# Kernel tuning notes

Measured on AMD Instinct MI355X. Metric: run time of the kernel, lower is better.

## Reference

```python
import jax, jax.numpy as jnp
import numpy as np

D, H, KVH, HD, FF = 768, 12, 4, 64, 2048
N_REP = H // KVH
EPS = 1e-6


def rmsnorm(x, w):
    # Faithful to source: norm = ||x|| * n^{-1/2}; eps added to norm (not inside sqrt)
    norm = jnp.sqrt(jnp.sum(x * x, axis=-1, keepdims=True)) * (x.shape[-1] ** -0.5)
    return w * x / (norm + EPS)


def rope_tables(seq_len, head_dim, base=10000.0):
    inv_freq = 1.0 / (base ** (np.arange(0, head_dim, 2, dtype=np.float32) / head_dim))
    t = np.arange(seq_len, dtype=np.float32)
    freqs = np.einsum('i,j->ij', t, inv_freq)  # [S, HD/2]
    emb = np.concatenate([freqs, freqs], axis=-1)  # [S, HD]
    return jnp.asarray(np.cos(emb)), jnp.asarray(np.sin(emb))


def rotate_half(x):
    h = x.shape[-1] // 2
    return jnp.concatenate([-x[..., h:], x[..., :h]], axis=-1)


def setup_inputs() -> dict:
    key = jax.random.key(0)
    ks = jax.random.split(key, 9)
    s = 0.02
    return {
        'x': jax.random.normal(ks[0], (2, 2048, D), jnp.float32),
        'Wq': jax.random.normal(ks[1], (H * HD, D), jnp.float32) * s,
        'Wk': jax.random.normal(ks[2], (KVH * HD, D), jnp.float32) * s,
        'Wv': jax.random.normal(ks[3], (KVH * HD, D), jnp.float32) * s,
        'Wo': jax.random.normal(ks[4], (D, H * HD), jnp.float32) * s,
        'Wgate': jax.random.normal(ks[5], (FF, D), jnp.float32) * s,
        'Wup': jax.random.normal(ks[6], (FF, D), jnp.float32) * s,
        'Wdown': jax.random.normal(ks[7], (D, FF), jnp.float32) * s,
        'g1': jnp.ones((D,), jnp.float32),
        'g2': jnp.ones((D,), jnp.float32),
    }


def reference(x, Wq, Wk, Wv, Wo, Wgate, Wup, Wdown, g1, g2):
    B, S, _ = x.shape
    # ---- attention sublayer (pre-norm) ----
    xn = rmsnorm(x, g1)
    q = (xn @ Wq.T).reshape(B, S, H, HD).transpose(0, 2, 1, 3)      # [B,H,S,HD]
    k = (xn @ Wk.T).reshape(B, S, KVH, HD).transpose(0, 2, 1, 3)    # [B,KVH,S,HD]
    v = (xn @ Wv.T).reshape(B, S, KVH, HD).transpose(0, 2, 1, 3)
    cos, sin = rope_tables(S, HD)                                   # [S,HD]
    q = q * cos + rotate_half(q) * sin
    k = k * cos + rotate_half(k) * sin
    # repeat kv heads to match q heads
    k = jnp.repeat(k, N_REP, axis=1)                                # [B,H,S,HD]
    v = jnp.repeat(v, N_REP, axis=1)
    scores = jnp.einsum('bhqd,bhkd->bhqk', q, k) / jnp.sqrt(jnp.float32(HD))
    causal = jnp.tril(jnp.ones((S, S), bool))
    scores = jnp.where(causal, scores, jnp.finfo(scores.dtype).min)
    attn = jax.nn.softmax(scores, axis=-1)
    out = jnp.einsum('bhqk,bhkd->bhqd', attn, v)                    # [B,H,S,HD]
    out = out.transpose(0, 2, 1, 3).reshape(B, S, H * HD) @ Wo.T
    x = x + out
    # ---- SwiGLU FFN sublayer (pre-norm) ----
    xn2 = rmsnorm(x, g2)
    ff = (jax.nn.silu(xn2 @ Wgate.T) * (xn2 @ Wup.T)) @ Wdown.T
    return x + ff
```

## Files before the change

kernel.cpp:

```cpp
#include <hip/hip_runtime.h>
#include <hip/hip_bf16.h>
#include <math.h>

typedef __bf16 bf16;
typedef __attribute__((ext_vector_type(8))) __bf16 bf16x8;
typedef __attribute__((ext_vector_type(4))) __bf16 bf16x4;
typedef __attribute__((ext_vector_type(4))) float f32x4;

#define MFMA16(a,b,c) __builtin_amdgcn_mfma_f32_16x16x32_bf16(a,b,c,0,0,0)

#define BATCH 2
#define SEQ   2048
#define DMODEL 768
#define NH    12
#define NKV   4
#define NREP  3
#define HD    64
#define FFDIM 2048
#define ROWS  (BATCH*SEQ)

#define QSCALE 0.18033688011112042f
#define LOG2E  1.4426950408889634f

__device__ __forceinline__ void gl2lds16(const bf16* g, bf16* l) {
  __builtin_amdgcn_global_load_lds(
      (const __attribute__((address_space(1))) void*)g,
      (__attribute__((address_space(3))) void*)l, 16, 0, 0);
}

struct Cvt7 { const float* s[7]; bf16* d[7]; int n[7]; };
__global__ __launch_bounds__(256) void cvt_all_kernel(Cvt7 c) {
  int seg = blockIdx.y;
  const float* __restrict__ src = c.s[seg];
  bf16* __restrict__ dst = c.d[seg];
  int n = c.n[seg];
  int stride = gridDim.x * 256;
  for (int i = blockIdx.x * 256 + threadIdx.x; i < n; i += stride)
    dst[i] = (bf16)src[i];
}

__global__ __launch_bounds__(256) void rmsnorm_kernel(const float* __restrict__ x,
    const float* __restrict__ g, bf16* __restrict__ out) {
  int row = blockIdx.x;
  const float* xr = x + (size_t)row * DMODEL;
  int t = threadIdx.x;
  float v0 = xr[t], v1 = xr[t + 256], v2 = xr[t + 512];
  float ss = v0 * v0 + v1 * v1 + v2 * v2;
  #pragma unroll
  for (int off = 32; off; off >>= 1) ss += __shfl_xor(ss, off, 64);
  __shared__ float red[4];
  if ((t & 63) == 0) red[t >> 6] = ss;
  __syncthreads();
  float total = red[0] + red[1] + red[2] + red[3];
  float norm = sqrtf(total) * 0.03608439182435161f;
  float sc = 1.0f / (norm + 1e-6f);
  bf16* orow = out + (size_t)row * DMODEL;
  orow[t]       = (bf16)(g[t]       * v0 * sc);
  orow[t + 256] = (bf16)(g[t + 256] * v1 * sc);
  orow[t + 512] = (bf16)(g[t + 512] * v2 * sc);
}

template<bool RES, typename OUTT>
__global__ __launch_bounds__(256) void gemm_bt64_kernel(const bf16* __restrict__ A,
    const bf16* __restrict__ B, OUTT* __restrict__ C, const float* __restrict__ R,
    int N, int K) {
  __shared__ __align__(16) bf16 At[64 * 32];
  __shared__ __align__(16) bf16 Bt[128 * 32];
  int t = threadIdx.x;
  int lane = t & 63;
  int wave = t >> 6;
  int l15 = lane & 15, lq = lane >> 4;
  int wrow = (wave >> 1) * 32, wcol = (wave & 1) * 64;
  int row0 = blockIdx.y * 64;
  int col0 = blockIdx.x * 128;
  int srow = t >> 2, sseg = (t & 3) * 8;
  const bf16* Ag0 = A + (size_t)(row0 + srow) * K + sseg;
  const bf16* Bg0 = B + (size_t)(col0 + srow) * K + sseg;
  const bf16* Bg1 = Bg0 + (size_t)64 * K;
  bf16* Al0 = At + t * 8;
  bf16* Bl0 = Bt + t * 8;
  bf16* Bl1 = Bt + 2048 + t * 8;

  f32x4 zero = {0.f, 0.f, 0.f, 0.f};
  f32x4 acc[2][4];
  #pragma unroll
  for (int m = 0; m < 2; ++m)
    #pragma unroll
    for (int n = 0; n < 4; ++n) acc[m][n] = zero;

  for (int k0 = 0; k0 < K; k0 += 32) {
    __syncthreads();
    gl2lds16(Ag0 + k0, Al0);
    gl2lds16(Bg0 + k0, Bl0);
    gl2lds16(Bg1 + k0, Bl1);
    __syncthreads();
    bf16x8 af[2], bf[4];
    #pragma unroll
    for (int m = 0; m < 2; ++m)
      af[m] = *(const bf16x8*)(At + (wrow + m * 16 + l15) * 32 + lq * 8);
    #pragma unroll
    for (int n = 0; n < 4; ++n)
      bf[n] = *(const bf16x8*)(Bt + (wcol + n * 16 + l15) * 32 + lq * 8);
    #pragma unroll
    for (int m = 0; m < 2; ++m)
      #pragma unroll
      for (int n = 0; n < 4; ++n)
        acc[m][n] = MFMA16(af[m], bf[n], acc[m][n]);
  }
  #pragma unroll
  for (int m = 0; m < 2; ++m)
    #pragma unroll
    for (int n = 0; n < 4; ++n)
      #pragma unroll
      for (int r = 0; r < 4; ++r) {
        size_t idx = (size_t)(row0 + wrow + m * 16 + lq * 4 + r) * N
                   + (col0 + wcol + n * 16 + l15);
        float v = acc[m][n][r];
        if (RES) v += R[idx];
        C[idx] = (OUTT)v;
      }
}

__global__ __launch_bounds__(256) void gemm_gu_kernel(const bf16* __restrict__ A,
    const bf16* __restrict__ Wg, const bf16* __restrict__ Wu, bf16* __restrict__ H) {
  __shared__ __align__(16) bf16 At[128 * 32];
  __shared__ __align__(16) bf16 Bgt[64 * 32];
  __shared__ __align__(16) bf16 But[64 * 32];
  const int K = DMODEL;
  int t = threadIdx.x;
  int lane = t & 63, wave = t >> 6;
  int l15 = lane & 15, lq = lane >> 4;
  int wrow = (wave >> 1) * 64, wcol = (wave & 1) * 32;
  int row0 = blockIdx.y * 128;
  int col0 = blockIdx.x * 64;
  int srow = t >> 2, sseg = (t & 3) * 8;
  const bf16* Ag0 = A + (size_t)(row0 + srow) * K + sseg;
  const bf16* Ag1 = Ag0 + (size_t)64 * K;
  const bf16* Gg = Wg + (size_t)(col0 + srow) * K + sseg;
  const bf16* Ug = Wu + (size_t)(col0 + srow) * K + sseg;
  bf16* Al0 = At + t * 8;
  bf16* Al1 = At + 2048 + t * 8;
  bf16* Bgd = Bgt + t * 8;
  bf16* Bud = But + t * 8;

  f32x4 zero = {0.f, 0.f, 0.f, 0.f};
  f32x4 ag[4][2], au[4][2];
  #pragma unroll
  for (int m = 0; m < 4; ++m)
    #pragma unroll
    for (int n = 0; n < 2; ++n) { ag[m][n] = zero; au[m][n] = zero; }

  for (int k0 = 0; k0 < K; k0 += 32) {
    __syncthreads();
    gl2lds16(Ag0 + k0, Al0);
    gl2lds16(Ag1 + k0, Al1);
    gl2lds16(Gg + k0, Bgd);
    gl2lds16(Ug + k0, Bud);
    __syncthreads();
    bf16x8 af[4], bg[2], bu[2];
    #pragma unroll
    for (int m = 0; m < 4; ++m)
      af[m] = *(const bf16x8*)(At + (wrow + m * 16 + l15) * 32 + lq * 8);
    #pragma unroll
    for (int n = 0; n < 2; ++n) {
      bg[n] = *(const bf16x8*)(Bgt + (wcol + n * 16 + l15) * 32 + lq * 8);
      bu[n] = *(const bf16x8*)(But + (wcol + n * 16 + l15) * 32 + lq * 8);
    }
    #pragma unroll
    for (int m = 0; m < 4; ++m)
      #pragma unroll
      for (int n = 0; n < 2; ++n) {
        ag[m][n] = MFMA16(af[m], bg[n], ag[m][n]);
        au[m][n] = MFMA16(af[m], bu[n], au[m][n]);
      }
  }
  #pragma unroll
  for (int m = 0; m < 4; ++m)
    #pragma unroll
    for (int n = 0; n < 2; ++n)
      #pragma unroll
      for (int r = 0; r < 4; ++r) {
        int row = row0 + wrow + m * 16 + lq * 4 + r;
        int col = col0 + wcol + n * 16 + l15;
        float g = ag[m][n][r], u = au[m][n][r];
        float sg = g / (1.f + __builtin_amdgcn_exp2f(-g * LOG2E));
        H[(size_t)row * FFDIM + col] = (bf16)(sg * u);
      }
}

__global__ __launch_bounds__(64) void rope_kernel(const bf16* __restrict__ qkv,
    bf16* __restrict__ Qh, bf16* __restrict__ Kh, bf16* __restrict__ Vt) {
  int token = blockIdx.x;
  int b = token >> 11, s = token & (SEQ - 1);
  int d = threadIdx.x;
  int j = d & 31;
  float inv = expf(-(float)j * (9.210340371976184f / 32.0f));
  float ang = (float)s * inv;
  float c = cosf(ang), si = sinf(ang);
  float sgn = (d < 32) ? -1.f : 1.f;
  const bf16* qr = qkv + (size_t)token * 1280;
  #pragma unroll
  for (int h = 0; h < NH; ++h) {
    float v = (float)qr[h * 64 + d];
    float other = (float)qr[h * 64 + (d ^ 32)];
    Qh[((size_t)(b * NH + h) * SEQ + s) * 64 + d] = (bf16)((v * c + sgn * other * si) * QSCALE);
  }
  #pragma unroll
  for (int hk = 0; hk < NKV; ++hk) {
    float v = (float)qr[768 + hk * 64 + d];
    float other = (float)qr[768 + hk * 64 + (d ^ 32)];
    Kh[((size_t)(b * NKV + hk) * SEQ + s) * 64 + d] = (bf16)(v * c + sgn * other * si);
    float vv = (float)qr[1024 + hk * 64 + d];
    Vt[((size_t)(b * NKV + hk) * 64 + d) * SEQ + s] = (bf16)vv;
  }
}

__global__ __launch_bounds__(256) void attn_kernel(const bf16* __restrict__ Qh,
    const bf16* __restrict__ Kh, const bf16* __restrict__ Vt, bf16* __restrict__ out) {
  __shared__ __align__(16) bf16 Kl0[64 * 32];
  __shared__ __align__(16) bf16 Kl1[64 * 32];
  __shared__ __align__(16) bf16 Vl0[64 * 32];
  __shared__ __align__(16) bf16 Vl1[64 * 32];
  __shared__ __align__(16) bf16 P[4][16 * 80];

  int idx = blockIdx.x;
  int qt = 31 - (idx / 24);
  int bh = idx % 24;
  int q0blk = qt * 64;
  int b = bh / NH, h = bh % NH;
  int kvh = h / NREP;
  int t = threadIdx.x;
  int lane = t & 63, wave = t >> 6;
  int l15 = lane & 15, lq = lane >> 4;
  int qw = q0blk + wave * 16;
  const bf16* Qb = Qh + (size_t)(b * NH + h) * SEQ * 64;
  const bf16* Kb = Kh + (size_t)(b * NKV + kvh) * SEQ * 64;
  const bf16* Vb = Vt + (size_t)(b * NKV + kvh) * 64 * SEQ;

  bf16x8 bq0 = *(const bf16x8*)(Qb + (size_t)(qw + l15) * 64 + lq * 8);
  bf16x8 bq1 = *(const bf16x8*)(Qb + (size_t)(qw + l15) * 64 + 32 + lq * 8);

  const bf16* Kg = Kb + (size_t)(t >> 2) * 64 + (t & 3) * 8;
  const bf16* Vg = Vb + (size_t)(t >> 2) * SEQ + (t & 3) * 8;
  bf16* Kl0d = Kl0 + t * 8;
  bf16* Kl1d = Kl1 + t * 8;
  bf16* Vl0d = Vl0 + t * 8;
  bf16* Vl1d = Vl1 + t * 8;
  bf16* Pw = P[wave];
  int Pwq = l15 * 80, lq8 = lq * 8, lq4 = lq * 4;

  f32x4 zero = {0.f, 0.f, 0.f, 0.f};
  f32x4 o[4];
  o[0] = zero; o[1] = zero; o[2] = zero; o[3] = zero;
  float l_r = 0.f;

  for (int k0 = 0; k0 <= q0blk + 63; k0 += 64) {
    __syncthreads();
    gl2lds16(Kg + (size_t)k0 * 64, Kl0d);
    gl2lds16(Kg + (size_t)k0 * 64 + 32, Kl1d);
    gl2lds16(Vg + k0, Vl0d);
    gl2lds16(Vg + k0 + 32, Vl1d);
    __syncthreads();
    f32x4 s[4];
    #pragma unroll
    for (int c = 0; c < 4; ++c) {
      bf16x8 ak0 = *(const bf16x8*)(Kl0 + (c * 16 + l15) * 32 + lq8);
      bf16x8 ak1 = *(const bf16x8*)(Kl1 + (c * 16 + l15) * 32 + lq8);
      s[c] = zero;
      s[c] = MFMA16(ak0, bq0, s[c]);
      s[c] = MFMA16(ak1, bq1, s[c]);
    }
    if (k0 + 63 > qw) {
      int qmk = qw + l15 - k0 - lq4;
      #pragma unroll
      for (int c = 0; c < 4; ++c)
        #pragma unroll
        for (int r = 0; r < 4; ++r)
          if (c * 16 + r > qmk) s[c][r] = -INFINITY;
    }
    #pragma unroll
    for (int c = 0; c < 4; ++c) {
      bf16x4 pe;
      #pragma unroll
      for (int r = 0; r < 4; ++r) {
        float e = __builtin_amdgcn_exp2f(s[c][r]);
        l_r += e;
        pe[r] = (bf16)e;
      }
      *(bf16x4*)(Pw + Pwq + c * 16 + lq4) = pe;
    }
    bf16x8 bp0 = *(const bf16x8*)(Pw + Pwq + lq8);
    bf16x8 bp1 = *(const bf16x8*)(Pw + Pwq + 32 + lq8);
    #pragma unroll
    for (int n = 0; n < 4; ++n) {
      bf16x8 av0 = *(const bf16x8*)(Vl0 + (n * 16 + l15) * 32 + lq8);
      bf16x8 av1 = *(const bf16x8*)(Vl1 + (n * 16 + l15) * 32 + lq8);
      o[n] = MFMA16(av0, bp0, o[n]);
      o[n] = MFMA16(av1, bp1, o[n]);
    }
  }
  float lt = l_r;
  lt += __shfl_xor(lt, 16, 64);
  lt += __shfl_xor(lt, 32, 64);
  float inv = 1.f / lt;
  int q = qw + l15;
  bf16* orow = out + (size_t)(b * SEQ + q) * DMODEL + h * 64;
  #pragma unroll
  for (int n = 0; n < 4; ++n) {
    bf16x4 po;
    #pragma unroll
    for (int r = 0; r < 4; ++r) po[r] = (bf16)(o[n][r] * inv);
    *(bf16x4*)(orow + n * 16 + lq4) = po;
  }
}

extern "C" void kernel_launch(void* const* d_in, const int* in_sizes, int n_in,
                              void* d_out, int out_size, void* d_ws, size_t ws_size,
                              hipStream_t stream) {
  const float* x     = (const float*)d_in[0];
  const float* Wq    = (const float*)d_in[1];
  const float* Wk    = (const float*)d_in[2];
  const float* Wv    = (const float*)d_in[3];
  const float* Wo    = (const float*)d_in[4];
  const float* Wgate = (const float*)d_in[5];
  const float* Wup   = (const float*)d_in[6];
  const float* Wdown = (const float*)d_in[7];
  const float* g1    = (const float*)d_in[8];
  const float* g2    = (const float*)d_in[9];
  float* out = (float*)d_out;

  char* ws = (char*)d_ws;
  size_t off = 0;
  auto alloc = [&](size_t bytes) { size_t o = off; off += (bytes + 255) & ~(size_t)255; return o; };
  size_t o_Wo   = alloc((size_t)768 * 768 * 2);
  size_t o_Wgu  = alloc((size_t)4096 * 768 * 2);
  size_t o_Wdn  = alloc((size_t)768 * 2048 * 2);
  size_t o_x1   = alloc((size_t)4096 * 768 * 4);
  size_t o_H    = alloc((size_t)4096 * 2048 * 2);
  size_t o_xn   = alloc((size_t)4096 * 768 * 2);
  size_t o_Wcat = alloc((size_t)1280 * 768 * 2);
  size_t arena  = alloc((size_t)4096 * 4096 * 2);
  size_t o_qkv  = arena;
  size_t o_Qh   = o_qkv + (size_t)4096 * 1280 * 2;
  size_t o_Kh   = o_Qh + (size_t)2 * 12 * 2048 * 64 * 2;
  size_t o_Vt   = o_Kh + (size_t)2 * 4 * 2048 * 64 * 2;
  size_t o_ao   = o_Vt + (size_t)2 * 4 * 64 * 2048 * 2;
  if (ws_size < off) return;

  bf16* bWo   = (bf16*)(ws + o_Wo);
  bf16* bWgu  = (bf16*)(ws + o_Wgu);
  bf16* bWdn  = (bf16*)(ws + o_Wdn);
  float* fx1  = (float*)(ws + o_x1);
  bf16* bH    = (bf16*)(ws + o_H);
  bf16* bxn   = (bf16*)(ws + o_xn);
  bf16* bWcat = (bf16*)(ws + o_Wcat);
  bf16* bqkv  = (bf16*)(ws + o_qkv);
  bf16* bQh   = (bf16*)(ws + o_Qh);
  bf16* bKh   = (bf16*)(ws + o_Kh);
  bf16* bVt   = (bf16*)(ws + o_Vt);
  bf16* bao   = (bf16*)(ws + o_ao);

  Cvt7 c;
  c.s[0] = Wq;    c.d[0] = bWcat;              c.n[0] = 768 * 768;
  c.s[1] = Wk;    c.d[1] = bWcat + 768 * 768;  c.n[1] = 256 * 768;
  c.s[2] = Wv;    c.d[2] = bWcat + 1024 * 768; c.n[2] = 256 * 768;
  c.s[3] = Wo;    c.d[3] = bWo;                c.n[3] = 768 * 768;
  c.s[4] = Wgate; c.d[4] = bWgu;               c.n[4] = 2048 * 768;
  c.s[5] = Wup;   c.d[5] = bWgu + 2048 * 768;  c.n[5] = 2048 * 768;
  c.s[6] = Wdown; c.d[6] = bWdn;               c.n[6] = 768 * 2048;
  cvt_all_kernel<<<dim3(256, 7), 256, 0, stream>>>(c);

  rmsnorm_kernel<<<4096, 256, 0, stream>>>(x, g1, bxn);
  gemm_bt64_kernel<false, bf16><<<dim3(10, 64), 256, 0, stream>>>(bxn, bWcat, bqkv, nullptr, 1280, 768);
  rope_kernel<<<4096, 64, 0, stream>>>(bqkv, bQh, bKh, bVt);
  attn_kernel<<<dim3(768), 256, 0, stream>>>(bQh, bKh, bVt, bao);
  gemm_bt64_kernel<true, float><<<dim3(6, 64), 256, 0, stream>>>(bao, bWo, fx1, x, 768, 768);

  rmsnorm_kernel<<<4096, 256, 0, stream>>>(fx1, g2, bxn);
  gemm_gu_kernel<<<dim3(32, 32), 256, 0, stream>>>(bxn, bWgu, bWgu + 2048 * 768, bH);
  gemm_bt64_kernel<true, float><<<dim3(6, 64), 256, 0, stream>>>(bH, bWdn, out, fx1, 768, 2048);
}
```

Measured before the change: 273.2 us.

## Fuse weight conversion into GEMMs and RoPE into QKV GEMM epilogue

Removes the separate fp32-to-bf16 weight conversion kernel by having each GEMM load fp32 weights into registers, pack them to bf16 and store them to LDS, with a one-step register prefetch. The QKV projection now applies RoPE (using a precomputed cos/sin table) and writes Q, K and transposed V directly in its epilogue, eliminating the intermediate qkv buffer and the separate rope kernel. This trades fewer launches and intermediate traffic for fp32 weight reads repeated by every row block and synchronous LDS stores in place of async global-to-LDS loads.

```diff
diff --git a/kernel.cpp b/kernel.cpp
--- a/kernel.cpp
+++ b/kernel.cpp
@@ -28,15 +28,20 @@
       (__attribute__((address_space(3))) void*)l, 16, 0, 0);
 }
 
-struct Cvt7 { const float* s[7]; bf16* d[7]; int n[7]; };
-__global__ __launch_bounds__(256) void cvt_all_kernel(Cvt7 c) {
-  int seg = blockIdx.y;
-  const float* __restrict__ src = c.s[seg];
-  bf16* __restrict__ dst = c.d[seg];
-  int n = c.n[seg];
-  int stride = gridDim.x * 256;
-  for (int i = blockIdx.x * 256 + threadIdx.x; i < n; i += stride)
-    dst[i] = (bf16)src[i];
+__device__ __forceinline__ bf16x8 pack8(f32x4 a, f32x4 b) {
+  bf16x8 o;
+  o[0] = (bf16)a[0]; o[1] = (bf16)a[1]; o[2] = (bf16)a[2]; o[3] = (bf16)a[3];
+  o[4] = (bf16)b[0]; o[5] = (bf16)b[1]; o[6] = (bf16)b[2]; o[7] = (bf16)b[3];
+  return o;
+}
+
+__global__ __launch_bounds__(256) void rope_tab_kernel(float* __restrict__ tab) {
+  int id = blockIdx.x * 256 + threadIdx.x;
+  int j = id >> 11, s = id & 2047;
+  float inv = expf(-(float)j * (9.210340371976184f / 32.0f));
+  float ang = (float)s * inv;
+  tab[id] = cosf(ang);
+  tab[65536 + id] = sinf(ang);
 }
 
 __global__ __launch_bounds__(256) void rmsnorm_kernel(const float* __restrict__ x,
@@ -61,8 +66,8 @@
 }
 
 template<bool RES, typename OUTT>
-__global__ __launch_bounds__(256) void gemm_bt64_kernel(const bf16* __restrict__ A,
-    const bf16* __restrict__ B, OUTT* __restrict__ C, const float* __restrict__ R,
+__global__ __launch_bounds__(256) void gemm_bt64f_kernel(const bf16* __restrict__ A,
+    const float* __restrict__ Bf, OUTT* __restrict__ C, const float* __restrict__ R,
     int N, int K) {
   __shared__ __align__(16) bf16 At[64 * 32];
   __shared__ __align__(16) bf16 Bt[128 * 32];
@@ -75,12 +80,15 @@
   int col0 = blockIdx.x * 128;
   int srow = t >> 2, sseg = (t & 3) * 8;
   const bf16* Ag0 = A + (size_t)(row0 + srow) * K + sseg;
-  const bf16* Bg0 = B + (size_t)(col0 + srow) * K + sseg;
-  const bf16* Bg1 = Bg0 + (size_t)64 * K;
+  const float* Bg0 = Bf + (size_t)(col0 + srow) * K + sseg;
+  const float* Bg1 = Bg0 + (size_t)64 * K;
   bf16* Al0 = At + t * 8;
   bf16* Bl0 = Bt + t * 8;
   bf16* Bl1 = Bt + 2048 + t * 8;
 
+  f32x4 b0a = *(const f32x4*)(Bg0), b0b = *(const f32x4*)(Bg0 + 4);
+  f32x4 b1a = *(const f32x4*)(Bg1), b1b = *(const f32x4*)(Bg1 + 4);
+
   f32x4 zero = {0.f, 0.f, 0.f, 0.f};
   f32x4 acc[2][4];
   #pragma unroll
@@ -91,21 +99,25 @@
   for (int k0 = 0; k0 < K; k0 += 32) {
     __syncthreads();
     gl2lds16(Ag0 + k0, Al0);
-    gl2lds16(Bg0 + k0, Bl0);
-    gl2lds16(Bg1 + k0, Bl1);
-    __syncthreads();
-    bf16x8 af[2], bf[4];
+    *(bf16x8*)Bl0 = pack8(b0a, b0b);
+    *(bf16x8*)Bl1 = pack8(b1a, b1b);
+    if (k0 + 32 < K) {
+      b0a = *(const f32x4*)(Bg0 + k0 + 32); b0b = *(const f32x4*)(Bg0 + k0 + 36);
+      b1a = *(const f32x4*)(Bg1 + k0 + 32); b1b = *(const f32x4*)(Bg1 + k0 + 36);
+    }
+    __syncthreads();
+    bf16x8 af[2], bfr[4];
     #pragma unroll
     for (int m = 0; m < 2; ++m)
       af[m] = *(const bf16x8*)(At + (wrow + m * 16 + l15) * 32 + lq * 8);
     #pragma unroll
     for (int n = 0; n < 4; ++n)
-      bf[n] = *(const bf16x8*)(Bt + (wcol + n * 16 + l15) * 32 + lq * 8);
+      bfr[n] = *(const bf16x8*)(Bt + (wcol + n * 16 + l15) * 32 + lq * 8);
     #pragma unroll
     for (int m = 0; m < 2; ++m)
       #pragma unroll
       for (int n = 0; n < 4; ++n)
-        acc[m][n] = MFMA16(af[m], bf[n], acc[m][n]);
+        acc[m][n] = MFMA16(af[m], bfr[n], acc[m][n]);
   }
   #pragma unroll
   for (int m = 0; m < 2; ++m)
@@ -121,8 +133,132 @@
       }
 }
 
+__global__ __launch_bounds__(256) void gemm_qkv_kernel(const bf16* __restrict__ A,
+    const float* __restrict__ Wq, const float* __restrict__ Wk, const float* __restrict__ Wv,
+    const float* __restrict__ tab, bf16* __restrict__ Qh, bf16* __restrict__ Kh,
+    bf16* __restrict__ Vt) {
+  __shared__ __align__(16) bf16 At[64 * 32];
+  __shared__ __align__(16) bf16 Bt[128 * 32];
+  const int K = DMODEL;
+  int t = threadIdx.x;
+  int lane = t & 63, wave = t >> 6;
+  int l15 = lane & 15, lq = lane >> 4;
+  int wrow = (wave >> 1) * 32, wcol = (wave & 1) * 64;
+  int row0 = blockIdx.y * 64;
+  int col0 = blockIdx.x * 128;
+  int srow = t >> 2, sseg = (t & 3) * 8;
+
+  const float* Bsrc; int brow;
+  if (col0 < 768)       { Bsrc = Wq; brow = col0; }
+  else if (col0 < 1024) { Bsrc = Wk; brow = col0 - 768; }
+  else                  { Bsrc = Wv; brow = col0 - 1024; }
+
+  const bf16* Ag0 = A + (size_t)(row0 + srow) * K + sseg;
+  const float* Bg0 = Bsrc + (size_t)(brow + srow) * K + sseg;
+  const float* Bg1 = Bg0 + (size_t)64 * K;
+  bf16* Al0 = At + t * 8;
+  bf16* Bl0 = Bt + t * 8;
+  bf16* Bl1 = Bt + 2048 + t * 8;
+
+  f32x4 b0a = *(const f32x4*)(Bg0), b0b = *(const f32x4*)(Bg0 + 4);
+  f32x4 b1a = *(const f32x4*)(Bg1), b1b = *(const f32x4*)(Bg1 + 4);
+
+  f32x4 zero = {0.f, 0.f, 0.f, 0.f};
+  f32x4 acc[2][4];
+  #pragma unroll
+  for (int m = 0; m < 2; ++m)
+    #pragma unroll
+    for (int n = 0; n < 4; ++n) acc[m][n] = zero;
+
+  for (int k0 = 0; k0 < K; k0 += 32) {
+    __syncthreads();
+    gl2lds16(Ag0 + k0, Al0);
+    *(bf16x8*)Bl0 = pack8(b0a, b0b);
+    *(bf16x8*)Bl1 = pack8(b1a, b1b);
+    if (k0 + 32 < K) {
+      b0a = *(const f32x4*)(Bg0 + k0 + 32); b0b = *(const f32x4*)(Bg0 + k0 + 36);
+      b1a = *(const f32x4*)(Bg1 + k0 + 32); b1b = *(const f32x4*)(Bg1 + k0 + 36);
+    }
+    __syncthreads();
+    bf16x8 af[2], bfr[4];
+    #pragma unroll
+    for (int m = 0; m < 2; ++m)
+      af[m] = *(const bf16x8*)(At + (wrow + m * 16 + l15) * 32 + lq * 8);
+    #pragma unroll
+    for (int n = 0; n < 4; ++n)
+      bfr[n] = *(const bf16x8*)(Bt + (wcol + n * 16 + l15) * 32 + lq * 8);
+    #pragma unroll
+    for (int m = 0; m < 2; ++m)
+      #pragma unroll
+      for (int n = 0; n < 4; ++n)
+        acc[m][n] = MFMA16(af[m], bfr[n], acc[m][n]);
+  }
+
+  int b = row0 >> 11;
+  int s0 = (row0 & 2047) + wrow + lq * 4;
+  int colw = col0 + wcol;
+  if (colw < 768) {
+    int h = colw >> 6;
+    f32x4 cv[2][2], sv[2][2];
+    #pragma unroll
+    for (int m = 0; m < 2; ++m)
+      #pragma unroll
+      for (int jh = 0; jh < 2; ++jh) {
+        const float* cp = tab + (jh * 16 + l15) * 2048 + s0 + m * 16;
+        cv[m][jh] = *(const f32x4*)cp;
+        sv[m][jh] = *(const f32x4*)(cp + 65536);
+      }
+    #pragma unroll
+    for (int m = 0; m < 2; ++m)
+      #pragma unroll
+      for (int n = 0; n < 4; ++n) {
+        float sgn = (n < 2) ? -1.f : 1.f;
+        #pragma unroll
+        for (int r = 0; r < 4; ++r) {
+          float c = cv[m][n & 1][r], si = sv[m][n & 1][r];
+          float rp = (acc[m][n][r] * c + sgn * acc[m][n ^ 2][r] * si) * QSCALE;
+          Qh[((size_t)(b * NH + h) * SEQ + s0 + m * 16 + r) * 64 + n * 16 + l15] = (bf16)rp;
+        }
+      }
+  } else if (colw < 1024) {
+    int kh = (colw - 768) >> 6;
+    f32x4 cv[2][2], sv[2][2];
+    #pragma unroll
+    for (int m = 0; m < 2; ++m)
+      #pragma unroll
+      for (int jh = 0; jh < 2; ++jh) {
+        const float* cp = tab + (jh * 16 + l15) * 2048 + s0 + m * 16;
+        cv[m][jh] = *(const f32x4*)cp;
+        sv[m][jh] = *(const f32x4*)(cp + 65536);
+      }
+    #pragma unroll
+    for (int m = 0; m < 2; ++m)
+      #pragma unroll
+      for (int n = 0; n < 4; ++n) {
+        float sgn = (n < 2) ? -1.f : 1.f;
+        #pragma unroll
+        for (int r = 0; r < 4; ++r) {
+          float c = cv[m][n & 1][r], si = sv[m][n & 1][r];
+          float rp = acc[m][n][r] * c + sgn * acc[m][n ^ 2][r] * si;
+          Kh[((size_t)(b * NKV + kh) * SEQ + s0 + m * 16 + r) * 64 + n * 16 + l15] = (bf16)rp;
+        }
+      }
+  } else {
+    int vh = (colw - 1024) >> 6;
+    #pragma unroll
+    for (int m = 0; m < 2; ++m)
+      #pragma unroll
+      for (int n = 0; n < 4; ++n) {
+        bf16x4 pv;
+        #pragma unroll
+        for (int r = 0; r < 4; ++r) pv[r] = (bf16)acc[m][n][r];
+        *(bf16x4*)(Vt + ((size_t)(b * NKV + vh) * 64 + n * 16 + l15) * SEQ + s0 + m * 16) = pv;
+      }
+  }
+}
+
 __global__ __launch_bounds__(256) void gemm_gu_kernel(const bf16* __restrict__ A,
-    const bf16* __restrict__ Wg, const bf16* __restrict__ Wu, bf16* __restrict__ H) {
+    const float* __restrict__ Wg, const float* __restrict__ Wu, bf16* __restrict__ H) {
   __shared__ __align__(16) bf16 At[128 * 32];
   __shared__ __align__(16) bf16 Bgt[64 * 32];
   __shared__ __align__(16) bf16 But[64 * 32];
@@ -136,13 +272,16 @@
   int srow = t >> 2, sseg = (t & 3) * 8;
   const bf16* Ag0 = A + (size_t)(row0 + srow) * K + sseg;
   const bf16* Ag1 = Ag0 + (size_t)64 * K;
-  const bf16* Gg = Wg + (size_t)(col0 + srow) * K + sseg;
-  const bf16* Ug = Wu + (size_t)(col0 + srow) * K + sseg;
+  const float* Gg = Wg + (size_t)(col0 + srow) * K + sseg;
+  const float* Ug = Wu + (size_t)(col0 + srow) * K + sseg;
   bf16* Al0 = At + t * 8;
   bf16* Al1 = At + 2048 + t * 8;
   bf16* Bgd = Bgt + t * 8;
   bf16* Bud = But + t * 8;
 
+  f32x4 ga = *(const f32x4*)(Gg), gb = *(const f32x4*)(Gg + 4);
+  f32x4 ua = *(const f32x4*)(Ug), ub = *(const f32x4*)(Ug + 4);
+
   f32x4 zero = {0.f, 0.f, 0.f, 0.f};
   f32x4 ag[4][2], au[4][2];
   #pragma unroll
@@ -154,8 +293,12 @@
     __syncthreads();
     gl2lds16(Ag0 + k0, Al0);
     gl2lds16(Ag1 + k0, Al1);
-    gl2lds16(Gg + k0, Bgd);
-    gl2lds16(Ug + k0, Bud);
+    *(bf16x8*)Bgd = pack8(ga, gb);
+    *(bf16x8*)Bud = pack8(ua, ub);
+    if (k0 + 32 < K) {
+      ga = *(const f32x4*)(Gg + k0 + 32); gb = *(const f32x4*)(Gg + k0 + 36);
+      ua = *(const f32x4*)(Ug + k0 + 32); ub = *(const f32x4*)(Ug + k0 + 36);
+    }
     __syncthreads();
     bf16x8 af[4], bg[2], bu[2];
     #pragma unroll
@@ -186,33 +329,6 @@
         float sg = g / (1.f + __builtin_amdgcn_exp2f(-g * LOG2E));
         H[(size_t)row * FFDIM + col] = (bf16)(sg * u);
       }
-}
-
-__global__ __launch_bounds__(64) void rope_kernel(const bf16* __restrict__ qkv,
-    bf16* __restrict__ Qh, bf16* __restrict__ Kh, bf16* __restrict__ Vt) {
-  int token = blockIdx.x;
-  int b = token >> 11, s = token & (SEQ - 1);
-  int d = threadIdx.x;
-  int j = d & 31;
-  float inv = expf(-(float)j * (9.210340371976184f / 32.0f));
-  float ang = (float)s * inv;
-  float c = cosf(ang), si = sinf(ang);
-  float sgn = (d < 32) ? -1.f : 1.f;
-  const bf16* qr = qkv + (size_t)token * 1280;
-  #pragma unroll
-  for (int h = 0; h < NH; ++h) {
-    float v = (float)qr[h * 64 + d];
-    float other = (float)qr[h * 64 + (d ^ 32)];
-    Qh[((size_t)(b * NH + h) * SEQ + s) * 64 + d] = (bf16)((v * c + sgn * other * si) * QSCALE);
-  }
-  #pragma unroll
-  for (int hk = 0; hk < NKV; ++hk) {
-    float v = (float)qr[768 + hk * 64 + d];
-    float other = (float)qr[768 + hk * 64 + (d ^ 32)];
-    Kh[((size_t)(b * NKV + hk) * SEQ + s) * 64 + d] = (bf16)(v * c + sgn * other * si);
-    float vv = (float)qr[1024 + hk * 64 + d];
-    Vt[((size_t)(b * NKV + hk) * 64 + d) * SEQ + s] = (bf16)vv;
-  }
 }
 
 __global__ __launch_bounds__(256) void attn_kernel(const bf16* __restrict__ Qh,
@@ -332,51 +448,33 @@
   char* ws = (char*)d_ws;
   size_t off = 0;
   auto alloc = [&](size_t bytes) { size_t o = off; off += (bytes + 255) & ~(size_t)255; return o; };
-  size_t o_Wo   = alloc((size_t)768 * 768 * 2);
-  size_t o_Wgu  = alloc((size_t)4096 * 768 * 2);
-  size_t o_Wdn  = alloc((size_t)768 * 2048 * 2);
-  size_t o_x1   = alloc((size_t)4096 * 768 * 4);
-  size_t o_H    = alloc((size_t)4096 * 2048 * 2);
-  size_t o_xn   = alloc((size_t)4096 * 768 * 2);
-  size_t o_Wcat = alloc((size_t)1280 * 768 * 2);
-  size_t arena  = alloc((size_t)4096 * 4096 * 2);
-  size_t o_qkv  = arena;
-  size_t o_Qh   = o_qkv + (size_t)4096 * 1280 * 2;
-  size_t o_Kh   = o_Qh + (size_t)2 * 12 * 2048 * 64 * 2;
-  size_t o_Vt   = o_Kh + (size_t)2 * 4 * 2048 * 64 * 2;
-  size_t o_ao   = o_Vt + (size_t)2 * 4 * 64 * 2048 * 2;
+  size_t o_tab = alloc((size_t)2 * 32 * 2048 * 4);
+  size_t o_x1  = alloc((size_t)4096 * 768 * 4);
+  size_t o_H   = alloc((size_t)4096 * 2048 * 2);
+  size_t o_xn  = alloc((size_t)4096 * 768 * 2);
+  size_t o_Qh  = alloc((size_t)2 * 12 * 2048 * 64 * 2);
+  size_t o_Kh  = alloc((size_t)2 * 4 * 2048 * 64 * 2);
+  size_t o_Vt  = alloc((size_t)2 * 4 * 64 * 2048 * 2);
+  size_t o_ao  = alloc((size_t)4096 * 768 * 2);
   if (ws_size < off) return;
 
-  bf16* bWo   = (bf16*)(ws + o_Wo);
-  bf16* bWgu  = (bf16*)(ws + o_Wgu);
-  bf16* bWdn  = (bf16*)(ws + o_Wdn);
+  float* tab  = (float*)(ws + o_tab);
   float* fx1  = (float*)(ws + o_x1);
   bf16* bH    = (bf16*)(ws + o_H);
   bf16* bxn   = (bf16*)(ws + o_xn);
-  bf16* bWcat = (bf16*)(ws + o_Wcat);
-  bf16* bqkv  = (bf16*)(ws + o_qkv);
   bf16* bQh   = (bf16*)(ws + o_Qh);
   bf16* bKh   = (bf16*)(ws + o_Kh);
   bf16* bVt   = (bf16*)(ws + o_Vt);
   bf16* bao   = (bf16*)(ws + o_ao);
 
-  Cvt7 c;
-  c.s[0] = Wq;    c.d[0] = bWcat;              c.n[0] = 768 * 768;
-  c.s[1] = Wk;    c.d[1] = bWcat + 768 * 768;  c.n[1] = 256 * 768;
-  c.s[2] = Wv;    c.d[2] = bWcat + 1024 * 768; c.n[2] = 256 * 768;
-  c.s[3] = Wo;    c.d[3] = bWo;                c.n[3] = 768 * 768;
-  c.s[4] = Wgate; c.d[4] = bWgu;               c.n[4] = 2048 * 768;
-  c.s[5] = Wup;   c.d[5] = bWgu + 2048 * 768;  c.n[5] = 2048 * 768;
-  c.s[6] = Wdown; c.d[6] = bWdn;               c.n[6] = 768 * 2048;
-  cvt_all_kernel<<<dim3(256, 7), 256, 0, stream>>>(c);
+  rope_tab_kernel<<<256, 256, 0, stream>>>(tab);
 
   rmsnorm_kernel<<<4096, 256, 0, stream>>>(x, g1, bxn);
-  gemm_bt64_kernel<false, bf16><<<dim3(10, 64), 256, 0, stream>>>(bxn, bWcat, bqkv, nullptr, 1280, 768);
-  rope_kernel<<<4096, 64, 0, stream>>>(bqkv, bQh, bKh, bVt);
+  gemm_qkv_kernel<<<dim3(10, 64), 256, 0, stream>>>(bxn, Wq, Wk, Wv, tab, bQh, bKh, bVt);
   attn_kernel<<<dim3(768), 256, 0, stream>>>(bQh, bKh, bVt, bao);
-  gemm_bt64_kernel<true, float><<<dim3(6, 64), 256, 0, stream>>>(bao, bWo, fx1, x, 768, 768);
+  gemm_bt64f_kernel<true, float><<<dim3(6, 64), 256, 0, stream>>>(bao, Wo, fx1, x, 768, 768);
 
   rmsnorm_kernel<<<4096, 256, 0, stream>>>(fx1, g2, bxn);
-  gemm_gu_kernel<<<dim3(32, 32), 256, 0, stream>>>(bxn, bWgu, bWgu + 2048 * 768, bH);
-  gemm_bt64_kernel<true, float><<<dim3(6, 64), 256, 0, stream>>>(bH, bWdn, out, fx1, 768, 2048);
-}
+  gemm_gu_kernel<<<dim3(32, 32), 256, 0, stream>>>(bxn, Wgate, Wup, bH);
+  gemm_bt64f_kernel<true, float><<<dim3(6, 64), 256, 0, stream>>>(bH, Wdown, out, fx1, 768, 2048);
+}
```

Result: no change. 268.3 us (-1.8%).
